# Kernel optimization log

Hardware: AMD Instinct MI355X
Metric: run time of the kernel (lower is better)

Reference implementation:

```python
import jax, jax.numpy as jnp
import numpy as np

N, C, H, W = 4, 256, 64, 64
K, G, PAD, STRIDE, DIL = 3, 8, 1, 1, 1
GC = C // G      # channels per group
P = K * K        # sampling points per group
HIN, WIN = H + 2 * PAD, W + 2 * PAD
BN_EPS = 1e-5
LN_EPS = 1e-5


def setup_inputs():
    key = jax.random.key(0)
    ks = jax.random.split(key, 8)
    f32 = jnp.float32
    return {
        "x": jax.random.normal(ks[0], (N, C, H, W), dtype=f32),
        "w_in": jax.random.normal(ks[1], (C, C), dtype=f32) * 0.05,
        "b_in": jnp.zeros((C,), f32),
        "w_dw": jax.random.normal(ks[2], (C, 1, K, K), dtype=f32) * 0.1,
        "b_dw": jnp.zeros((C,), f32),
        "ln_g": jnp.ones((C,), f32), "ln_b": jnp.zeros((C,), f32),
        "w_off": jax.random.normal(ks[3], (C, G * P * 2), dtype=f32) * 0.01,
        "b_off": jax.random.normal(ks[4], (G * P * 2,), dtype=f32) * 0.01,
        "w_mask": jax.random.normal(ks[5], (C, G * P), dtype=f32) * 0.01,
        "b_mask": jnp.zeros((G * P,), f32),
        "w_out": jax.random.normal(ks[6], (C, C), dtype=f32) * 0.05,
        "b_out": jnp.zeros((C,), f32),
        "bn_g": jnp.ones((C,), f32), "bn_b": jnp.zeros((C,), f32),
        "bn_mean": jnp.zeros((C,), f32), "bn_var": jnp.ones((C,), f32),
    }


def _bilinear(img, grid):
    # img: (B, Cc, Hh, Ww); grid: (B, S, P, 2) normalized to [-1,1],
    # matches F.grid_sample(mode='bilinear', padding_mode='zeros', align_corners=False)
    B, Cc, Hh, Ww = img.shape
    gx = (grid[..., 0] + 1.0) * 0.5 * Ww - 0.5
    gy = (grid[..., 1] + 1.0) * 0.5 * Hh - 0.5
    x0 = jnp.floor(gx)
    y0 = jnp.floor(gy)
    wx = gx - x0
    wy = gy - y0
    flat = img.reshape(B, Cc, Hh * Ww)

    def tap(xi, yi, wgt):
        valid = (xi >= 0) & (xi <= Ww - 1) & (yi >= 0) & (yi <= Hh - 1)
        idx = (jnp.clip(yi, 0, Hh - 1) * Ww + jnp.clip(xi, 0, Ww - 1)).astype(jnp.int32)
        v = jax.vmap(lambda im, ix: im[:, ix])(flat, idx)   # (B, Cc, S, P)
        return v * (wgt * valid.astype(img.dtype))[:, None]

    return (tap(x0, y0, (1 - wx) * (1 - wy)) + tap(x0 + 1, y0, wx * (1 - wy))
            + tap(x0, y0 + 1, (1 - wx) * wy) + tap(x0 + 1, y0 + 1, wx * wy))


def _forward(x, w_in, b_in, w_dw, b_dw, ln_g, ln_b, w_off, b_off,
             w_mask, b_mask, w_out, b_out, bn_g, bn_b, bn_mean, bn_var):
    xl = jnp.transpose(x, (0, 2, 3, 1))                      # (N,H,W,C) channels-last
    x_proj = xl @ w_in + b_in                                # input_proj
    # depthwise conv + LayerNorm + GELU feature branch for offset/mask prediction
    dw = jax.lax.conv_general_dilated(
        x, w_dw, (1, 1), ((PAD, PAD), (PAD, PAD)),
        feature_group_count=C, dimension_numbers=("NCHW", "OIHW", "NCHW"))
    dw = jnp.transpose(dw + b_dw[None, :, None, None], (0, 2, 3, 1))
    mu = dw.mean(-1, keepdims=True)
    var = ((dw - mu) ** 2).mean(-1, keepdims=True)
    dw = (dw - mu) * jax.lax.rsqrt(var + LN_EPS) * ln_g + ln_b
    x1 = jax.nn.gelu(dw, approximate=False)
    offset = x1 @ w_off + b_off                              # (N,H,W,G*P*2)
    mask = jax.nn.softmax((x1 @ w_mask + b_mask).reshape(N, H, W, G, P), axis=-1)
    # reference points + dilation kernel grid, normalized to padded input, (x,y) order
    ry = ((DIL * (K - 1)) // 2 + 0.5 + jnp.arange(H, dtype=x.dtype) * STRIDE) / HIN
    rx = ((DIL * (K - 1)) // 2 + 0.5 + jnp.arange(W, dtype=x.dtype) * STRIDE) / WIN
    ref = jnp.stack(jnp.broadcast_arrays(rx[None, :], ry[:, None]), axis=-1)  # (H,W,2)
    px = (jnp.arange(K, dtype=x.dtype) * DIL - (DIL * (K - 1)) // 2) / WIN
    py = (jnp.arange(K, dtype=x.dtype) * DIL - (DIL * (K - 1)) // 2) / HIN
    gx, gy = jnp.meshgrid(px, py, indexing="ij")             # kw-major flattening as in DCNv3
    kgrid = jnp.stack([gx, gy], -1).reshape(P, 2)
    norm = jnp.array([WIN, HIN], dtype=x.dtype)
    loc = (ref[None, :, :, None, None, :] + kgrid[None, None, None, None, :, :]
           + offset.reshape(N, H, W, G, P, 2) / norm)        # (N,H,W,G,P,2), offset_scale=1
    sgrid = 2.0 * loc - 1.0
    # group-split padded value tensor and deformable sampling
    xp = jnp.pad(x_proj, ((0, 0), (PAD, PAD), (PAD, PAD), (0, 0)))
    img = jnp.transpose(xp, (0, 3, 1, 2)).reshape(N * G, GC, HIN, WIN)
    sg = jnp.transpose(sgrid.reshape(N, H * W, G, P, 2), (0, 2, 1, 3, 4)).reshape(N * G, H * W, P, 2)
    sampled = _bilinear(img, sg)                             # (N*G, GC, H*W, P)
    m = jnp.transpose(mask.reshape(N, H * W, G, P), (0, 2, 1, 3)).reshape(N * G, 1, H * W, P)
    agg = (sampled * m).sum(-1)                              # (N*G, GC, H*W)
    y = jnp.transpose(agg.reshape(N, C, H * W), (0, 2, 1)).reshape(N, H, W, C)
    y = y @ w_out + b_out                                    # output_proj
    y = jnp.transpose(y, (0, 3, 1, 2))                       # back to NCHW
    y = (y - bn_mean[None, :, None, None]) * jax.lax.rsqrt(bn_var + BN_EPS)[None, :, None, None]
    y = y * bn_g[None, :, None, None] + bn_b[None, :, None, None]
    return y * jax.nn.sigmoid(y)                             # SiLU (Conv.default_act)


def reference(x, w_in, b_in, w_dw, b_dw, ln_g, ln_b, w_off, b_off,
              w_mask, b_mask, w_out, b_out, bn_g, bn_b, bn_mean, bn_var):
    return _forward(x, w_in, b_in, w_dw, b_dw, ln_g, ln_b, w_off, b_off,
                    w_mask, b_mask, w_out, b_out, bn_g, bn_b, bn_mean, bn_var)
```

## Files before the change

### kernel.cpp

```cpp
#include <hip/hip_runtime.h>
#include <math.h>

#define NB   4
#define CCH  256
#define HH   64
#define WW   64
#define GG   8
#define GCH  32
#define PP   9
#define HIN  66
#define WIN  66
#define HWSZ 4096
#define NPIX 16384

#define XP_ELEMS   (NB*HIN*WIN*CCH)
#define WINT_ELEMS (CCH*CCH)
#define WOUTT_ELEMS (CCH*CCH)
#define WOMT_ELEMS (216*CCH)
#define OFF_ELEMS  (NPIX*144)
#define MSK_ELEMS  (NPIX*72)

typedef __attribute__((ext_vector_type(8))) short bf16x8;
typedef __attribute__((ext_vector_type(4))) float f32x4;

__device__ __forceinline__ unsigned short f2bf(float f) {
    unsigned int u = __float_as_uint(f);
    unsigned int r = (u + 0x7FFFu + ((u >> 16) & 1u)) >> 16;
    return (unsigned short)r;
}
__device__ __forceinline__ float bf2f(unsigned short s) {
    return __uint_as_float(((unsigned int)s) << 16);
}

#define SDW_STRIDE 258

__global__ __launch_bounds__(256) void k_prep(
    const float* __restrict__ w_in, const float* __restrict__ w_off,
    const float* __restrict__ w_mask, const float* __restrict__ w_out,
    unsigned short* __restrict__ win_t, unsigned short* __restrict__ womt,
    unsigned short* __restrict__ wout_t, unsigned short* __restrict__ xp)
{
    const int gtid = blockIdx.x * 256 + threadIdx.x;
    const int STRIDE = 128 * 256;
    for (int i = gtid; i < 252928; i += STRIDE) {
        if (i < 65536) {
            int n = i & 255, k = i >> 8;
            win_t[n * 256 + k] = f2bf(w_in[i]);
        } else if (i < 131072) {
            int j = i - 65536;
            int n = j & 255, k = j >> 8;
            wout_t[n * 256 + k] = f2bf(w_out[j]);
        } else if (i < 186368) {
            int j = i - 131072;
            int k = j / 216, col = j - k * 216;
            float v = (col < 144) ? w_off[k * 144 + col]
                                  : w_mask[k * 72 + col - 144];
            womt[col * 256 + k] = f2bf(v);
        } else {
            int r = i - 186368;
            int seg = r >> 6, ln = r & 63;
            int n = seg / 260, rp = seg % 260;
            int h, w;
            if (rp < 66)       { h = 0;        w = rp; }
            else if (rp < 132) { h = 65;       w = rp - 66; }
            else if (rp < 196) { h = rp - 131; w = 0; }
            else               { h = rp - 195; w = 65; }
            uint2 z = make_uint2(0u, 0u);
            *(uint2*)&xp[(((size_t)n * HIN + h) * WIN + w) * CCH + ln * 4] = z;
        }
    }
}

__global__ __launch_bounds__(1024) void k_dw_fused(
    const float* __restrict__ x, const float* __restrict__ w_dw,
    const float* __restrict__ b_dw, const float* __restrict__ ln_g,
    const float* __restrict__ ln_b, const float* __restrict__ b_in,
    const unsigned short* __restrict__ win_t, const unsigned short* __restrict__ womt,
    const float* __restrict__ b_off, const float* __restrict__ b_mask,
    unsigned short* __restrict__ xp, float* __restrict__ off,
    float* __restrict__ msk)
{
    __shared__ unsigned short sdw[64 * SDW_STRIDE];
    __shared__ unsigned short sxr[64 * SDW_STRIDE];
    __shared__ float rr1[64][65];
    __shared__ float rr2[64][65];
    __shared__ float mu_s[64];
    __shared__ float rs_s[64];
    __shared__ float swdw[2304];
    __shared__ float sbdw[256];

    const int b = blockIdx.x;
    const int tid = threadIdx.x;
    const int h = b & 63;
    const int n = b >> 6;
    const int wave = __builtin_amdgcn_readfirstlane(tid >> 6);
    const int lane = tid & 63;
    const int grp  = lane >> 4;
    const int l16  = lane & 15;

    for (int i = tid; i < 2304; i += 1024) swdw[i] = w_dw[i];
    if (tid < 256) sbdw[tid] = b_dw[tid];
    __syncthreads();

    const float* xn = x + (size_t)n * CCH * HWSZ;
    const bool h0ok = (h > 0);
    const bool h2ok = (h < HH - 1);

    float s1q[4] = {0.f, 0.f, 0.f, 0.f};
    float s2q[4] = {0.f, 0.f, 0.f, 0.f};

#pragma unroll
    for (int it = 0; it < 4; it++) {
        const int c = it * 64 + wave * 4 + grp;
        const float* xr = xn + (size_t)c * HWSZ + h * WW + l16 * 4;
        float4 v1 = *(const float4*)xr;
        float4 v0 = h0ok ? *(const float4*)(xr - WW) : make_float4(0.f,0.f,0.f,0.f);
        float4 v2 = h2ok ? *(const float4*)(xr + WW) : make_float4(0.f,0.f,0.f,0.f);

        const float* wk = &swdw[c * 9];
        float accq[4];
        float bias = sbdw[c];
#pragma unroll
        for (int k = 0; k < 4; k++) accq[k] = bias;

#define CROW(v, wa, wb, wc)                                            \
        {                                                              \
            float wl = __shfl_up((v).w, 1);   if (l16 == 0)  wl = 0.f; \
            float wr = __shfl_down((v).x, 1); if (l16 == 15) wr = 0.f; \
            accq[0] += (wa) * wl    + (wb) * (v).x + (wc) * (v).y;     \
            accq[1] += (wa) * (v).x + (wb) * (v).y + (wc) * (v).z;     \
            accq[2] += (wa) * (v).y + (wb) * (v).z + (wc) * (v).w;     \
            accq[3] += (wa) * (v).z + (wb) * (v).w + (wc) * wr;        \
        }
        CROW(v0, wk[0], wk[1], wk[2]);
        CROW(v1, wk[3], wk[4], wk[5]);
        CROW(v2, wk[6], wk[7], wk[8]);
#undef CROW

        float xv[4] = {v1.x, v1.y, v1.z, v1.w};
#pragma unroll
        for (int k = 0; k < 4; k++) {
            s1q[k] += accq[k];
            s2q[k] += accq[k] * accq[k];
            sdw[(l16 * 4 + k) * SDW_STRIDE + c] = f2bf(accq[k]);
            sxr[(l16 * 4 + k) * SDW_STRIDE + c] = f2bf(xv[k]);
        }
    }

    {
        const int contrib = wave * 4 + grp;
#pragma unroll
        for (int k = 0; k < 4; k++) {
            rr1[l16 * 4 + k][contrib] = s1q[k];
            rr2[l16 * 4 + k][contrib] = s2q[k];
        }
    }
    __syncthreads();

    if (tid < 64) {
        float a1 = 0.f, a2 = 0.f;
#pragma unroll
        for (int q = 0; q < 64; q++) { a1 += rr1[tid][q]; a2 += rr2[tid][q]; }
        float mu = a1 * (1.0f / 256.0f);
        float var = a2 * (1.0f / 256.0f) - mu * mu;
        mu_s[tid] = mu;
        rs_s[tid] = rsqrtf(var + 1e-5f);
    }
    __syncthreads();

    {
        const int c0 = (tid & 63) * 4;
        float g4[4], b4[4];
#pragma unroll
        for (int i = 0; i < 4; i++) { g4[i] = ln_g[c0 + i]; b4[i] = ln_b[c0 + i]; }
#pragma unroll
        for (int pass = 0; pass < 4; pass++) {
            int w = wave + pass * 16;
            float mu = mu_s[w], rs = rs_s[w];
            unsigned short* row = &sdw[w * SDW_STRIDE + c0];
#pragma unroll
            for (int i = 0; i < 4; i++) {
                float v = (bf2f(row[i]) - mu) * rs * g4[i] + b4[i];
                row[i] = f2bf(0.5f * v * (1.0f + erff(v * 0.70710678118654752f)));
            }
        }
    }
    __syncthreads();

    const int r16  = lane & 15;
    const int quad = lane >> 4;
    const int wm   = wave >> 2;
    const int wn   = wave & 3;

#define LOAD_A(frag, basep, koff)                                   \
    {                                                               \
        const unsigned short* ap_ = (basep) + (koff);               \
        ((unsigned int*)&(frag))[0] = *(const unsigned int*)&ap_[0];\
        ((unsigned int*)&(frag))[1] = *(const unsigned int*)&ap_[2];\
        ((unsigned int*)&(frag))[2] = *(const unsigned int*)&ap_[4];\
        ((unsigned int*)&(frag))[3] = *(const unsigned int*)&ap_[6];\
    }

    {
        f32x4 acc[4];
#pragma unroll
        for (int i = 0; i < 4; i++) acc[i] = (f32x4){0.f, 0.f, 0.f, 0.f};
        const unsigned short* arow = &sxr[(wm * 16 + r16) * SDW_STRIDE];

#pragma unroll
        for (int k0 = 0; k0 < CCH; k0 += 32) {
            bf16x8 a;
            LOAD_A(a, arow, k0 + quad * 8);
#pragma unroll
            for (int i = 0; i < 4; i++) {
                int co = (wn * 4 + i) * 16 + r16;
                bf16x8 bfr = *(const bf16x8*)&win_t[(size_t)co * CCH + k0 + quad * 8];
                acc[i] = __builtin_amdgcn_mfma_f32_16x16x32_bf16(a, bfr, acc[i], 0, 0, 0);
            }
        }

        unsigned short* xprow = xp + (((size_t)n * HIN + (h + 1)) * WIN + 1) * CCH;
#pragma unroll
        for (int i = 0; i < 4; i++) {
            int co = (wn * 4 + i) * 16 + r16;
            float bias = b_in[co];
#pragma unroll
            for (int r = 0; r < 4; r++) {
                int w = wm * 16 + quad * 4 + r;
                xprow[(size_t)w * CCH + co] = f2bf(acc[i][r] + bias);
            }
        }
    }

    {
        f32x4 acc[4];
#pragma unroll
        for (int i = 0; i < 4; i++) acc[i] = (f32x4){0.f, 0.f, 0.f, 0.f};
        const unsigned short* arow = &sdw[(wm * 16 + r16) * SDW_STRIDE];

#pragma unroll
        for (int k0 = 0; k0 < CCH; k0 += 32) {
            bf16x8 a;
            LOAD_A(a, arow, k0 + quad * 8);
#pragma unroll
            for (int i = 0; i < 4; i++) {
                int col = (wn * 4 + i) * 16 + r16;
                int colc = (col < 216) ? col : 215;
                bf16x8 bfr = *(const bf16x8*)&womt[(size_t)colc * CCH + k0 + quad * 8];
                acc[i] = __builtin_amdgcn_mfma_f32_16x16x32_bf16(a, bfr, acc[i], 0, 0, 0);
            }
        }

        const int sbase = n * HWSZ + h * WW;
#pragma unroll
        for (int i = 0; i < 4; i++) {
            int col = (wn * 4 + i) * 16 + r16;
            if (col >= 216) continue;
            float bias = (col < 144) ? b_off[col] : b_mask[col - 144];
#pragma unroll
            for (int r = 0; r < 4; r++) {
                int w = wm * 16 + quad * 4 + r;
                int s = sbase + w;
                float v = acc[i][r] + bias;
                if (col < 144) off[(size_t)s * 144 + col] = v;
                else           msk[(size_t)s * 72 + col - 144] = v;
            }
        }
    }
#undef LOAD_A
}

__device__ __forceinline__ void acc8_tap(float* a, uint4 vv, float wgt) {
    a[0] += wgt * __uint_as_float(vv.x << 16);
    a[1] += wgt * __uint_as_float(vv.x & 0xffff0000u);
    a[2] += wgt * __uint_as_float(vv.y << 16);
    a[3] += wgt * __uint_as_float(vv.y & 0xffff0000u);
    a[4] += wgt * __uint_as_float(vv.z << 16);
    a[5] += wgt * __uint_as_float(vv.z & 0xffff0000u);
    a[6] += wgt * __uint_as_float(vv.w << 16);
    a[7] += wgt * __uint_as_float(vv.w & 0xffff0000u);
}

__global__ __launch_bounds__(512) void k_samp_out(
    const unsigned short* __restrict__ xp, const float* __restrict__ off,
    const float* __restrict__ msk, const unsigned short* __restrict__ wout_t,
    const float* __restrict__ b_out, const float* __restrict__ bn_g,
    const float* __restrict__ bn_b, const float* __restrict__ bn_mean,
    const float* __restrict__ bn_var, float* __restrict__ out)
{
    __shared__ int2   tco[2304];
    __shared__ float4 twt[2304];
    __shared__ unsigned short agg_l[32 * SDW_STRIDE];

    const int tid = threadIdx.x;
    const int s0 = blockIdx.x * 32;
    const int n = s0 >> 12;
    const int hw0 = s0 & 4095;

    if (tid < 256) {
        const int pix = tid >> 3, g = tid & 7;
        const int s = s0 + pix;
        const int hw = s & 4095;
        const int h = hw >> 6, w = hw & 63;
        const float* mskp = msk + (size_t)s * 72 + g * 9;
        const float* offp = off + (size_t)s * 144 + g * 18;
        float e[9];
        float mx = -1e30f;
#pragma unroll
        for (int p = 0; p < PP; p++) { e[p] = mskp[p]; mx = fmaxf(mx, e[p]); }
        float sum = 0.f;
#pragma unroll
        for (int p = 0; p < PP; p++) { e[p] = __expf(e[p] - mx); sum += e[p]; }
        float rs = 1.0f / sum;
#pragma unroll
        for (int p = 0; p < PP; p++) {
            float m = e[p] * rs;
            float ox = offp[p * 2], oy = offp[p * 2 + 1];
            int i = p / 3, j = p - i * 3;
            float fx = (float)(w + i) + ox;
            float fy = (float)(h + j) + oy;
            float x0f = floorf(fx), y0f = floorf(fy);
            int x0 = (int)x0f, y0 = (int)y0f;
            float wx = fx - x0f, wy = fy - y0f;
            float w00 = (1.f - wx) * (1.f - wy) * m;
            float w10 = wx * (1.f - wy) * m;
            float w01 = (1.f - wx) * wy * m;
            float w11 = wx * wy * m;
            int x1c = x0 + 1, y1c = y0 + 1;
            if (!((x0  >= 0) && (x0  < WIN))) { w00 = 0.f; w01 = 0.f; }
            if (!((x1c >= 0) && (x1c < WIN))) { w10 = 0.f; w11 = 0.f; }
            if (!((y0  >= 0) && (y0  < HIN))) { w00 = 0.f; w10 = 0.f; }
            if (!((y1c >= 0) && (y1c < HIN))) { w01 = 0.f; w11 = 0.f; }
            int cx0 = min(max(x0, 0), WIN - 1), cx1 = min(max(x1c, 0), WIN - 1);
            int cy0 = min(max(y0, 0), HIN - 1), cy1 = min(max(y1c, 0), HIN - 1);
            tco[tid * 9 + p] = make_int2(cx0 | (cx1 << 16), cy0 | (cy1 << 16));
            twt[tid * 9 + p] = make_float4(w00, w10, w01, w11);
        }
    }
    __syncthreads();

    const int l5 = tid & 31;
    const int g = l5 >> 2, c8 = l5 & 3;
    const unsigned short* base = xp + (size_t)n * HIN * WIN * CCH + g * GCH + c8 * 8;

#pragma unroll
    for (int pp = 0; pp < 2; pp++) {
        const int pix = pp * 16 + (tid >> 5);
        const int tbase = pix * 72 + g * 9;

        float a[8];
#pragma unroll
        for (int i = 0; i < 8; i++) a[i] = 0.f;

#pragma unroll
        for (int p = 0; p < PP; p++) {
            int2 cc = tco[tbase + p];
            float4 wt = twt[tbase + p];
            int cx0 = cc.x & 0xFFFF, cx1 = cc.x >> 16;
            int cy0 = cc.y & 0xFFFF, cy1 = cc.y >> 16;
            const unsigned short* r0 = base + (size_t)(cy0 * WIN) * CCH;
            const unsigned short* r1 = base + (size_t)(cy1 * WIN) * CCH;
            uint4 v00 = *(const uint4*)&r0[(size_t)cx0 * CCH];
            uint4 v10 = *(const uint4*)&r0[(size_t)cx1 * CCH];
            uint4 v01 = *(const uint4*)&r1[(size_t)cx0 * CCH];
            uint4 v11 = *(const uint4*)&r1[(size_t)cx1 * CCH];
            acc8_tap(a, v00, wt.x);
            acc8_tap(a, v10, wt.y);
            acc8_tap(a, v01, wt.z);
            acc8_tap(a, v11, wt.w);
        }

        unsigned int* dst = (unsigned int*)&agg_l[pix * SDW_STRIDE + g * GCH + c8 * 8];
        dst[0] = (unsigned int)f2bf(a[0]) | ((unsigned int)f2bf(a[1]) << 16);
        dst[1] = (unsigned int)f2bf(a[2]) | ((unsigned int)f2bf(a[3]) << 16);
        dst[2] = (unsigned int)f2bf(a[4]) | ((unsigned int)f2bf(a[5]) << 16);
        dst[3] = (unsigned int)f2bf(a[6]) | ((unsigned int)f2bf(a[7]) << 16);
    }
    __syncthreads();

    {
        const int wave = tid >> 6;
        const int lane = tid & 63;
        const int r16  = lane & 15;
        const int quad = lane >> 4;
        const int wm   = wave >> 2;
        const int wn   = wave & 3;

        f32x4 acc[4];
#pragma unroll
        for (int i = 0; i < 4; i++) acc[i] = (f32x4){0.f, 0.f, 0.f, 0.f};

        const unsigned short* arow = &agg_l[(wm * 16 + r16) * SDW_STRIDE];

#pragma unroll
        for (int k0 = 0; k0 < CCH; k0 += 32) {
            bf16x8 a;
            {
                const unsigned short* ap_ = arow + k0 + quad * 8;
                ((unsigned int*)&a)[0] = *(const unsigned int*)&ap_[0];
                ((unsigned int*)&a)[1] = *(const unsigned int*)&ap_[2];
                ((unsigned int*)&a)[2] = *(const unsigned int*)&ap_[4];
                ((unsigned int*)&a)[3] = *(const unsigned int*)&ap_[6];
            }
#pragma unroll
            for (int nt = 0; nt < 4; nt++) {
                int co = wn * 64 + nt * 16 + r16;
                bf16x8 bfr = *(const bf16x8*)&wout_t[(size_t)co * CCH + k0 + quad * 8];
                acc[nt] = __builtin_amdgcn_mfma_f32_16x16x32_bf16(a, bfr, acc[nt], 0, 0, 0);
            }
        }

#pragma unroll
        for (int nt = 0; nt < 4; nt++) {
            int co = wn * 64 + nt * 16 + r16;
            float mean = bn_mean[co];
            float rstd = rsqrtf(bn_var[co] + 1e-5f);
            float gg = bn_g[co], bb = bn_b[co], bo = b_out[co];
            int hwb = hw0 + wm * 16 + quad * 4;
            float tmp[4];
#pragma unroll
            for (int r = 0; r < 4; r++) {
                float y = acc[nt][r] + bo;
                float yh = (y - mean) * rstd * gg + bb;
                tmp[r] = yh / (1.0f + __expf(-yh));
            }
            float4 v = make_float4(tmp[0], tmp[1], tmp[2], tmp[3]);
            *(float4*)&out[((size_t)n * CCH + co) * HWSZ + hwb] = v;
        }
    }
}

extern "C" void kernel_launch(void* const* d_in, const int* in_sizes, int n_in,
                              void* d_out, int out_size, void* d_ws, size_t ws_size,
                              hipStream_t stream)
{
    const float* x       = (const float*)d_in[0];
    const float* w_in    = (const float*)d_in[1];
    const float* b_in    = (const float*)d_in[2];
    const float* w_dw    = (const float*)d_in[3];
    const float* b_dw    = (const float*)d_in[4];
    const float* ln_g    = (const float*)d_in[5];
    const float* ln_b    = (const float*)d_in[6];
    const float* w_off   = (const float*)d_in[7];
    const float* b_off   = (const float*)d_in[8];
    const float* w_mask  = (const float*)d_in[9];
    const float* b_mask  = (const float*)d_in[10];
    const float* w_out   = (const float*)d_in[11];
    const float* b_out   = (const float*)d_in[12];
    const float* bn_g    = (const float*)d_in[13];
    const float* bn_b    = (const float*)d_in[14];
    const float* bn_mean = (const float*)d_in[15];
    const float* bn_var  = (const float*)d_in[16];
    float* out = (float*)d_out;

    unsigned short* xp     = (unsigned short*)d_ws;
    unsigned short* win_t  = xp + XP_ELEMS;
    unsigned short* wout_t = win_t + WINT_ELEMS;
    unsigned short* womt   = wout_t + WOUTT_ELEMS;
    float* off = (float*)(womt + WOMT_ELEMS);
    float* msk = off + OFF_ELEMS;

    k_prep<<<dim3(128), 256, 0, stream>>>(w_in, w_off, w_mask, w_out,
                                          win_t, womt, wout_t, xp);
    k_dw_fused<<<dim3(256), 1024, 0, stream>>>(x, w_dw, b_dw, ln_g, ln_b, b_in,
                                               win_t, womt, b_off, b_mask,
                                               xp, off, msk);
    k_samp_out<<<dim3(512), 512, 0, stream>>>(xp, off, msk, wout_t, b_out,
                                              bn_g, bn_b, bn_mean, bn_var, out);
}
```

Baseline: 183.0 us.

## Stage depthwise input rows via async global-to-LDS double-buffered loads

The depthwise-conv prologue of the fused kernel now loads its three input rows per channel straight into a double-buffered LDS stage with global_load_lds. It issues the next channel chunk while computing the current one. Each lane now owns one pixel and processes two channels per chunk. This makes the LayerNorm partial-sum reduction smaller (16 contributors instead of 64). The aim is to hide global load latency and cut register pressure, at the cost of extra LDS footprint and per-lane 4-byte loads instead of float4, plus a possible race because there is no block barrier around the per-wave buffer reuse.

Result: faster. 178.3 us (-2.6%).

```diff
diff --git a/kernel.cpp b/kernel.cpp
--- a/kernel.cpp
+++ b/kernel.cpp
@@ -30,6 +30,12 @@
 }
 __device__ __forceinline__ float bf2f(unsigned short s) {
     return __uint_as_float(((unsigned int)s) << 16);
+}
+
+typedef const __attribute__((address_space(1))) void cgvoid;
+typedef __attribute__((address_space(3))) void lvoid;
+__device__ __forceinline__ void gload_lds4(const float* g, float* l) {
+    __builtin_amdgcn_global_load_lds((cgvoid*)g, (lvoid*)l, 4, 0, 0);
 }
 
 #define SDW_STRIDE 258
@@ -80,10 +86,11 @@
     unsigned short* __restrict__ xp, float* __restrict__ off,
     float* __restrict__ msk)
 {
+    __shared__ float xstage[2][32][3][64];
     __shared__ unsigned short sdw[64 * SDW_STRIDE];
     __shared__ unsigned short sxr[64 * SDW_STRIDE];
-    __shared__ float rr1[64][65];
-    __shared__ float rr2[64][65];
+    __shared__ float r1s[16][64];
+    __shared__ float r2s[16][64];
     __shared__ float mu_s[64];
     __shared__ float rs_s[64];
     __shared__ float swdw[2304];
@@ -95,8 +102,6 @@
     const int n = b >> 6;
     const int wave = __builtin_amdgcn_readfirstlane(tid >> 6);
     const int lane = tid & 63;
-    const int grp  = lane >> 4;
-    const int l16  = lane & 15;
 
     for (int i = tid; i < 2304; i += 1024) swdw[i] = w_dw[i];
     if (tid < 256) sbdw[tid] = b_dw[tid];
@@ -105,62 +110,83 @@
     const float* xn = x + (size_t)n * CCH * HWSZ;
     const bool h0ok = (h > 0);
     const bool h2ok = (h < HH - 1);
-
-    float s1q[4] = {0.f, 0.f, 0.f, 0.f};
-    float s2q[4] = {0.f, 0.f, 0.f, 0.f};
-
-#pragma unroll
-    for (int it = 0; it < 4; it++) {
-        const int c = it * 64 + wave * 4 + grp;
-        const float* xr = xn + (size_t)c * HWSZ + h * WW + l16 * 4;
-        float4 v1 = *(const float4*)xr;
-        float4 v0 = h0ok ? *(const float4*)(xr - WW) : make_float4(0.f,0.f,0.f,0.f);
-        float4 v2 = h2ok ? *(const float4*)(xr + WW) : make_float4(0.f,0.f,0.f,0.f);
-
-        const float* wk = &swdw[c * 9];
-        float accq[4];
-        float bias = sbdw[c];
-#pragma unroll
-        for (int k = 0; k < 4; k++) accq[k] = bias;
-
-#define CROW(v, wa, wb, wc)                                            \
-        {                                                              \
-            float wl = __shfl_up((v).w, 1);   if (l16 == 0)  wl = 0.f; \
-            float wr = __shfl_down((v).x, 1); if (l16 == 15) wr = 0.f; \
-            accq[0] += (wa) * wl    + (wb) * (v).x + (wc) * (v).y;     \
-            accq[1] += (wa) * (v).x + (wb) * (v).y + (wc) * (v).z;     \
-            accq[2] += (wa) * (v).y + (wb) * (v).z + (wc) * (v).w;     \
-            accq[3] += (wa) * (v).z + (wb) * (v).w + (wc) * wr;        \
-        }
-        CROW(v0, wk[0], wk[1], wk[2]);
-        CROW(v1, wk[3], wk[4], wk[5]);
-        CROW(v2, wk[6], wk[7], wk[8]);
-#undef CROW
-
-        float xv[4] = {v1.x, v1.y, v1.z, v1.w};
-#pragma unroll
-        for (int k = 0; k < 4; k++) {
-            s1q[k] += accq[k];
-            s2q[k] += accq[k] * accq[k];
-            sdw[(l16 * 4 + k) * SDW_STRIDE + c] = f2bf(accq[k]);
-            sxr[(l16 * 4 + k) * SDW_STRIDE + c] = f2bf(xv[k]);
-        }
-    }
-
-    {
-        const int contrib = wave * 4 + grp;
-#pragma unroll
-        for (int k = 0; k < 4; k++) {
-            rr1[l16 * 4 + k][contrib] = s1q[k];
-            rr2[l16 * 4 + k][contrib] = s2q[k];
-        }
-    }
+    const int d0 = h0ok ? -WW : 0;
+    const int d2 = h2ok ?  WW : 0;
+
+#define ISSUE(ck, bb)                                                   \
+    {                                                                   \
+        const int cA_ = (ck) * 32 + wave * 2;                           \
+        const float* gA_ = xn + (size_t)cA_ * HWSZ + h * WW + lane;     \
+        const float* gB_ = gA_ + HWSZ;                                  \
+        float* dA_ = &xstage[bb][wave * 2][0][0];                       \
+        float* dB_ = &xstage[bb][wave * 2 + 1][0][0];                   \
+        gload_lds4(gA_ + d0, dA_);                                      \
+        gload_lds4(gA_,      dA_ + 64);                                 \
+        gload_lds4(gA_ + d2, dA_ + 128);                                \
+        gload_lds4(gB_ + d0, dB_);                                      \
+        gload_lds4(gB_,      dB_ + 64);                                 \
+        gload_lds4(gB_ + d2, dB_ + 128);                                \
+    }
+
+    float s1 = 0.f, s2 = 0.f;
+
+    ISSUE(0, 0);
+#pragma unroll
+    for (int ck = 0; ck < 8; ck++) {
+        const int bb = ck & 1;
+        asm volatile("s_waitcnt vmcnt(0)" ::: "memory");
+        __builtin_amdgcn_sched_barrier(0);
+
+        if (!h0ok) {
+            xstage[bb][wave * 2][0][lane] = 0.f;
+            xstage[bb][wave * 2 + 1][0][lane] = 0.f;
+        }
+        if (!h2ok) {
+            xstage[bb][wave * 2][2][lane] = 0.f;
+            xstage[bb][wave * 2 + 1][2][lane] = 0.f;
+        }
+
+        if (ck < 7) ISSUE(ck + 1, bb ^ 1);
+
+#pragma unroll
+        for (int j = 0; j < 2; j++) {
+            const int c = ck * 32 + wave * 2 + j;
+            const int lc = wave * 2 + j;
+            float v0 = xstage[bb][lc][0][lane];
+            float v1 = xstage[bb][lc][1][lane];
+            float v2 = xstage[bb][lc][2][lane];
+
+            const float* wk = &swdw[c * 9];
+            float acc = sbdw[c];
+
+            float l0 = __shfl_up(v0, 1);   if (lane == 0)  l0 = 0.f;
+            float r0 = __shfl_down(v0, 1); if (lane == 63) r0 = 0.f;
+            acc += wk[0] * l0 + wk[1] * v0 + wk[2] * r0;
+
+            float l1 = __shfl_up(v1, 1);   if (lane == 0)  l1 = 0.f;
+            float r1 = __shfl_down(v1, 1); if (lane == 63) r1 = 0.f;
+            acc += wk[3] * l1 + wk[4] * v1 + wk[5] * r1;
+
+            float l2 = __shfl_up(v2, 1);   if (lane == 0)  l2 = 0.f;
+            float r2 = __shfl_down(v2, 1); if (lane == 63) r2 = 0.f;
+            acc += wk[6] * l2 + wk[7] * v2 + wk[8] * r2;
+
+            s1 += acc;
+            s2 += acc * acc;
+            sdw[lane * SDW_STRIDE + c] = f2bf(acc);
+            sxr[lane * SDW_STRIDE + c] = f2bf(v1);
+        }
+    }
+#undef ISSUE
+
+    r1s[wave][lane] = s1;
+    r2s[wave][lane] = s2;
     __syncthreads();
 
     if (tid < 64) {
         float a1 = 0.f, a2 = 0.f;
 #pragma unroll
-        for (int q = 0; q < 64; q++) { a1 += rr1[tid][q]; a2 += rr2[tid][q]; }
+        for (int q = 0; q < 16; q++) { a1 += r1s[q][tid]; a2 += r2s[q][tid]; }
         float mu = a1 * (1.0f / 256.0f);
         float var = a2 * (1.0f / 256.0f) - mu * mu;
         mu_s[tid] = mu;
```

## Split depthwise/LN/projection kernel into half-row blocks of 512 threads

Applied to the files above, without the earlier changes.

Each block of the fused depthwise-conv, LayerNorm and projection kernel now handles 32 pixels (half an image row) with 512 threads, instead of a full 64-pixel row with 1024 threads. The grid doubles to 512 blocks. The depthwise conv switches from float4-per-lane with 16-lane shuffles to one scalar per lane with 32-lane shuffles, plus explicit halo loads at the split seam. The aim is more, lighter blocks per CU for better occupancy and latency hiding. The cost is that every block rereads the full projection weights from global memory, so total weight traffic doubles, and the input loads lose their vector width.

Result: no change. 183.1 us (+0.0%).

```diff
diff --git a/kernel.cpp b/kernel.cpp
--- a/kernel.cpp
+++ b/kernel.cpp
@@ -71,7 +71,7 @@
     }
 }
 
-__global__ __launch_bounds__(1024) void k_dw_fused(
+__global__ __launch_bounds__(512) void k_dw_fused(
     const float* __restrict__ x, const float* __restrict__ w_dw,
     const float* __restrict__ b_dw, const float* __restrict__ ln_g,
     const float* __restrict__ ln_b, const float* __restrict__ b_in,
@@ -80,25 +80,26 @@
     unsigned short* __restrict__ xp, float* __restrict__ off,
     float* __restrict__ msk)
 {
-    __shared__ unsigned short sdw[64 * SDW_STRIDE];
-    __shared__ unsigned short sxr[64 * SDW_STRIDE];
-    __shared__ float rr1[64][65];
-    __shared__ float rr2[64][65];
-    __shared__ float mu_s[64];
-    __shared__ float rs_s[64];
+    __shared__ unsigned short sdw[32 * SDW_STRIDE];
+    __shared__ unsigned short sxr[32 * SDW_STRIDE];
+    __shared__ float r1s[16][32];
+    __shared__ float r2s[16][32];
+    __shared__ float mu_s[32];
+    __shared__ float rs_s[32];
     __shared__ float swdw[2304];
     __shared__ float sbdw[256];
 
     const int b = blockIdx.x;
     const int tid = threadIdx.x;
-    const int h = b & 63;
-    const int n = b >> 6;
+    const int n    = b >> 7;
+    const int h    = (b >> 1) & 63;
+    const int w0   = (b & 1) * 32;
     const int wave = __builtin_amdgcn_readfirstlane(tid >> 6);
     const int lane = tid & 63;
-    const int grp  = lane >> 4;
-    const int l16  = lane & 15;
-
-    for (int i = tid; i < 2304; i += 1024) swdw[i] = w_dw[i];
+    const int l    = lane & 31;
+    const int cpar = lane >> 5;
+
+    for (int i = tid; i < 2304; i += 512) swdw[i] = w_dw[i];
     if (tid < 256) sbdw[tid] = b_dw[tid];
     __syncthreads();
 
@@ -106,61 +107,59 @@
     const bool h0ok = (h > 0);
     const bool h2ok = (h < HH - 1);
 
-    float s1q[4] = {0.f, 0.f, 0.f, 0.f};
-    float s2q[4] = {0.f, 0.f, 0.f, 0.f};
-
-#pragma unroll
-    for (int it = 0; it < 4; it++) {
-        const int c = it * 64 + wave * 4 + grp;
-        const float* xr = xn + (size_t)c * HWSZ + h * WW + l16 * 4;
-        float4 v1 = *(const float4*)xr;
-        float4 v0 = h0ok ? *(const float4*)(xr - WW) : make_float4(0.f,0.f,0.f,0.f);
-        float4 v2 = h2ok ? *(const float4*)(xr + WW) : make_float4(0.f,0.f,0.f,0.f);
+    float s1 = 0.f, s2 = 0.f;
+
+#pragma unroll 4
+    for (int it = 0; it < 16; it++) {
+        const int c = it * 16 + wave * 2 + cpar;
+        const float* xc = xn + (size_t)c * HWSZ + h * WW + w0 + l;
+        float v0 = h0ok ? xc[-WW] : 0.f;
+        float v1 = xc[0];
+        float v2 = h2ok ? xc[WW] : 0.f;
 
         const float* wk = &swdw[c * 9];
-        float accq[4];
-        float bias = sbdw[c];
-#pragma unroll
-        for (int k = 0; k < 4; k++) accq[k] = bias;
-
-#define CROW(v, wa, wb, wc)                                            \
-        {                                                              \
-            float wl = __shfl_up((v).w, 1);   if (l16 == 0)  wl = 0.f; \
-            float wr = __shfl_down((v).x, 1); if (l16 == 15) wr = 0.f; \
-            accq[0] += (wa) * wl    + (wb) * (v).x + (wc) * (v).y;     \
-            accq[1] += (wa) * (v).x + (wb) * (v).y + (wc) * (v).z;     \
-            accq[2] += (wa) * (v).y + (wb) * (v).z + (wc) * (v).w;     \
-            accq[3] += (wa) * (v).z + (wb) * (v).w + (wc) * wr;        \
-        }
-        CROW(v0, wk[0], wk[1], wk[2]);
-        CROW(v1, wk[3], wk[4], wk[5]);
-        CROW(v2, wk[6], wk[7], wk[8]);
-#undef CROW
-
-        float xv[4] = {v1.x, v1.y, v1.z, v1.w};
-#pragma unroll
-        for (int k = 0; k < 4; k++) {
-            s1q[k] += accq[k];
-            s2q[k] += accq[k] * accq[k];
-            sdw[(l16 * 4 + k) * SDW_STRIDE + c] = f2bf(accq[k]);
-            sxr[(l16 * 4 + k) * SDW_STRIDE + c] = f2bf(xv[k]);
-        }
-    }
-
-    {
-        const int contrib = wave * 4 + grp;
-#pragma unroll
-        for (int k = 0; k < 4; k++) {
-            rr1[l16 * 4 + k][contrib] = s1q[k];
-            rr2[l16 * 4 + k][contrib] = s2q[k];
-        }
-    }
-    __syncthreads();
-
-    if (tid < 64) {
+        float acc = sbdw[c];
+
+        float lh0 = 0.f, lh1 = 0.f, lh2 = 0.f;
+        float rh0 = 0.f, rh1 = 0.f, rh2 = 0.f;
+        if (l == 0 && w0 > 0) {
+            lh1 = xc[-1];
+            if (h0ok) lh0 = xc[-1 - WW];
+            if (h2ok) lh2 = xc[-1 + WW];
+        }
+        if (l == 31 && w0 == 0) {
+            rh1 = xc[1];
+            if (h0ok) rh0 = xc[1 - WW];
+            if (h2ok) rh2 = xc[1 + WW];
+        }
+
+        float t;
+        t = __shfl_up(v0, 1);   float l0 = (l == 0)  ? lh0 : t;
+        t = __shfl_down(v0, 1); float r0 = (l == 31) ? rh0 : t;
+        acc += wk[0] * l0 + wk[1] * v0 + wk[2] * r0;
+
+        t = __shfl_up(v1, 1);   float l1 = (l == 0)  ? lh1 : t;
+        t = __shfl_down(v1, 1); float r1 = (l == 31) ? rh1 : t;
+        acc += wk[3] * l1 + wk[4] * v1 + wk[5] * r1;
+
+        t = __shfl_up(v2, 1);   float l2 = (l == 0)  ? lh2 : t;
+        t = __shfl_down(v2, 1); float r2 = (l == 31) ? rh2 : t;
+        acc += wk[6] * l2 + wk[7] * v2 + wk[8] * r2;
+
+        s1 += acc;
+        s2 += acc * acc;
+        sdw[l * SDW_STRIDE + c] = f2bf(acc);
+        sxr[l * SDW_STRIDE + c] = f2bf(v1);
+    }
+
+    r1s[wave * 2 + cpar][l] = s1;
+    r2s[wave * 2 + cpar][l] = s2;
+    __syncthreads();
+
+    if (tid < 32) {
         float a1 = 0.f, a2 = 0.f;
 #pragma unroll
-        for (int q = 0; q < 64; q++) { a1 += rr1[tid][q]; a2 += rr2[tid][q]; }
+        for (int q = 0; q < 16; q++) { a1 += r1s[q][tid]; a2 += r2s[q][tid]; }
         float mu = a1 * (1.0f / 256.0f);
         float var = a2 * (1.0f / 256.0f) - mu * mu;
         mu_s[tid] = mu;
@@ -175,7 +174,7 @@
         for (int i = 0; i < 4; i++) { g4[i] = ln_g[c0 + i]; b4[i] = ln_b[c0 + i]; }
 #pragma unroll
         for (int pass = 0; pass < 4; pass++) {
-            int w = wave + pass * 16;
+            int w = wave + pass * 8;
             float mu = mu_s[w], rs = rs_s[w];
             unsigned short* row = &sdw[w * SDW_STRIDE + c0];
 #pragma unroll
@@ -219,7 +218,7 @@
             }
         }
 
-        unsigned short* xprow = xp + (((size_t)n * HIN + (h + 1)) * WIN + 1) * CCH;
+        unsigned short* xprow = xp + (((size_t)n * HIN + (h + 1)) * WIN + 1 + w0) * CCH;
 #pragma unroll
         for (int i = 0; i < 4; i++) {
             int co = (wn * 4 + i) * 16 + r16;
@@ -251,7 +250,7 @@
             }
         }
 
-        const int sbase = n * HWSZ + h * WW;
+        const int sbase = n * HWSZ + h * WW + w0;
 #pragma unroll
         for (int i = 0; i < 4; i++) {
             int col = (wn * 4 + i) * 16 + r16;
@@ -462,9 +461,9 @@
 
     k_prep<<<dim3(128), 256, 0, stream>>>(w_in, w_off, w_mask, w_out,
                                           win_t, womt, wout_t, xp);
-    k_dw_fused<<<dim3(256), 1024, 0, stream>>>(x, w_dw, b_dw, ln_g, ln_b, b_in,
-                                               win_t, womt, b_off, b_mask,
-                                               xp, off, msk);
+    k_dw_fused<<<dim3(512), 512, 0, stream>>>(x, w_dw, b_dw, ln_g, ln_b, b_in,
+                                              win_t, womt, b_off, b_mask,
+                                              xp, off, msk);
     k_samp_out<<<dim3(512), 512, 0, stream>>>(xp, off, msk, wout_t, b_out,
                                               bn_g, bn_b, bn_mean, bn_var, out);
 }
```
